# Kernel optimization log

Measured on AMD Instinct MI355X. Metric: run time of the kernel, lower is better.

Reference implementation:

```python
import jax, jax.numpy as jnp
import numpy as np

B, L, V, DIN, H = 256, 256, 2048, 128, 256   # trees, leaves/tree, vocab, in_dim, mem_dim
NODES = 2 * L - 1                            # perfect binary tree, level-by-level layout
LEVELS = int(np.log2(L)) + 1                 # 9 levels: 256,128,...,1 nodes


def setup_inputs() -> dict:
    key = jax.random.key(0)
    ks = jax.random.split(key, 32)
    w = lambda k, shape: jax.random.normal(k, shape, jnp.float32) * 0.05
    inp = {
        "input_ids": jax.random.randint(ks[0], (B, NODES), 0, V),
        "emb": w(ks[1], (V, DIN)),
        # iou projections (i,o,u concatenated -> 3H)
        "Wioux": w(ks[2], (DIN, 3 * H)), "bioux": jnp.zeros((3 * H,), jnp.float32),
        "Wiouh1": w(ks[3], (H, 3 * H)), "biouh1": jnp.zeros((3 * H,), jnp.float32),
        "Wiouh2": w(ks[4], (H, 3 * H)), "biouh2": jnp.zeros((3 * H,), jnp.float32),
        # forget gates
        "Wfx": w(ks[5], (DIN, H)), "bfx": jnp.zeros((H,), jnp.float32),
        "Wfh11": w(ks[6], (H, H)), "bfh11": jnp.zeros((H,), jnp.float32),
        "Wfh12": w(ks[7], (H, H)), "bfh12": jnp.zeros((H,), jnp.float32),
        "Wfh21": w(ks[8], (H, H)), "bfh21": jnp.zeros((H,), jnp.float32),
        "Wfh22": w(ks[9], (H, H)), "bfh22": jnp.zeros((H,), jnp.float32),
        # classifier head
        "Wl1": w(ks[10], (H, 100)), "bl1": jnp.zeros((100,), jnp.float32),
        "Wl2": w(ks[11], (100, 1)), "bl2": jnp.zeros((1,), jnp.float32),
    }
    return inp


def reference(input_ids, emb, Wioux, bioux, Wiouh1, biouh1, Wiouh2, biouh2,
              Wfx, bfx, Wfh11, bfh11, Wfh12, bfh12, Wfh21, bfh21, Wfh22, bfh22,
              Wl1, bl1, Wl2, bl2):
    emb = emb.at[0].set(0.0)                 # padding_idx=0
    xemb = emb[input_ids]                    # [B, NODES, DIN]

    def cell(x, h1, h2, c1, c2):
        iou = (x @ Wioux + bioux) + (h1 @ Wiouh1 + biouh1) + (h2 @ Wiouh2 + biouh2)
        i, o, u = jnp.split(iou, 3, axis=-1)
        i, o, u = jax.nn.sigmoid(i), jax.nn.sigmoid(o), jnp.tanh(u)
        fx = x @ Wfx + bfx
        f0 = jax.nn.sigmoid((h1 @ Wfh11 + bfh11) + (h2 @ Wfh12 + bfh12) + fx)
        f1 = jax.nn.sigmoid((h1 @ Wfh21 + bfh21) + (h2 @ Wfh22 + bfh22) + fx)
        c = i * u + f0 * c1 + f1 * c2
        h = o * jnp.tanh(c)
        return h, c

    # leaves: zero child states
    z = jnp.zeros((B, L, H), jnp.float32)
    h, c = cell(xemb[:, :L], z, z, z, z)     # [B, L, H]

    off, n = 0, L
    for _ in range(LEVELS - 1):              # fixed small structural loop (8 iters)
        off += n
        n //= 2
        x = xemb[:, off:off + n]             # [B, n, DIN]
        h, c = cell(x, h[:, 0::2], h[:, 1::2], c[:, 0::2], c[:, 1::2])

    root_h = h[:, 0]                         # [B, H]
    hid = root_h @ Wl1 + bl1                 # linear1
    pred = (jax.nn.relu(hid) @ Wl2 + bl2)[..., 0]   # [B], arithmetic head (no softmax)
    return pred
```

## Files before the change

### kernel.cpp

```cpp
#include <hip/hip_runtime.h>
#include <math.h>

#define B_ 256
#define L_ 256
#define V_ 2048
#define DIN_ 128
#define H_ 256
#define NODES_ 511

typedef _Float16 half8 __attribute__((ext_vector_type(8)));
typedef float f32x4 __attribute__((ext_vector_type(4)));

__device__ __forceinline__ float sigm(float x) { return 1.f / (1.f + __expf(-x)); }
__device__ __forceinline__ float tanh_f(float x) {
    float xc = fminf(fmaxf(x, -15.f), 15.f);
    float e = __expf(2.f * xc);
    return (e - 1.f) / (e + 1.f);
}
__device__ __forceinline__ void gload16(const void* g, void* l) {
    __builtin_amdgcn_global_load_lds((const __attribute__((address_space(1))) unsigned int*)g,
                                     (__attribute__((address_space(3))) unsigned int*)l, 16, 0, 0);
}
template<int N> __device__ __forceinline__ void vwaitN() {
    asm volatile("s_waitcnt vmcnt(%0)" :: "i"(N) : "memory");
}

__global__ void build_WTh(_Float16* __restrict__ WTh,
    const float* __restrict__ Wiouh1, const float* __restrict__ Wfh11, const float* __restrict__ Wfh21,
    const float* __restrict__ Wiouh2, const float* __restrict__ Wfh12, const float* __restrict__ Wfh22)
{
    int e = blockIdx.x * 256 + threadIdx.x;
    int nn = e >> 9, k = e & 511;
    int g = nn >> 8, t = nn & 255;
    float v;
    if (k < 256) {
        v = (g < 3) ? Wiouh1[k * 768 + nn] : ((g == 3) ? Wfh11[k * 256 + t] : Wfh21[k * 256 + t]);
    } else {
        int kp = k - 256;
        v = (g < 3) ? Wiouh2[kp * 768 + nn] : ((g == 3) ? Wfh12[kp * 256 + t] : Wfh22[kp * 256 + t]);
    }
    WTh[e] = (_Float16)v;
}

__global__ __launch_bounds__(256) void build_table(float* __restrict__ tab, const float* __restrict__ emb,
    const float* __restrict__ Wioux, const float* __restrict__ Wfx,
    const float* __restrict__ bioux, const float* __restrict__ biouh1, const float* __restrict__ biouh2,
    const float* __restrict__ bfx, const float* __restrict__ bfh11, const float* __restrict__ bfh12,
    const float* __restrict__ bfh21, const float* __restrict__ bfh22)
{
    __shared__ float As[64][33];
    __shared__ float Ws[32][65];
    const int tid = threadIdx.x, tx = tid & 15, ty = tid >> 4;
    const int i0 = blockIdx.x * 64, c0 = blockIdx.y * 64;
    const int g = c0 >> 8;
    float acc[4][4];
    #pragma unroll
    for (int i = 0; i < 4; ++i)
        #pragma unroll
        for (int j = 0; j < 4; ++j) acc[i][j] = 0.f;

    for (int k0 = 0; k0 < 128; k0 += 32) {
        #pragma unroll
        for (int it = 0; it < 2; ++it) {
            int f = tid + it * 256;
            int row = f >> 3, kk = (f & 7) * 4;
            int gr = i0 + row;
            float4 av = (gr == 0) ? make_float4(0.f, 0.f, 0.f, 0.f)
                                  : *(const float4*)(emb + (size_t)gr * 128 + k0 + kk);
            As[row][kk] = av.x; As[row][kk + 1] = av.y; As[row][kk + 2] = av.z; As[row][kk + 3] = av.w;
            int k = f >> 4, cc = (f & 15) * 4;
            int col = c0 + cc;
            float4 wv = (g < 3) ? *(const float4*)(Wioux + (size_t)(k0 + k) * 768 + col)
                                : *(const float4*)(Wfx + (size_t)(k0 + k) * 256 + (col & 255));
            Ws[k][cc] = wv.x; Ws[k][cc + 1] = wv.y; Ws[k][cc + 2] = wv.z; Ws[k][cc + 3] = wv.w;
        }
        __syncthreads();
        #pragma unroll 8
        for (int k = 0; k < 32; ++k) {
            float a[4], w[4];
            #pragma unroll
            for (int i = 0; i < 4; ++i) a[i] = As[ty * 4 + i][k];
            #pragma unroll
            for (int j = 0; j < 4; ++j) w[j] = Ws[k][tx * 4 + j];
            #pragma unroll
            for (int i = 0; i < 4; ++i)
                #pragma unroll
                for (int j = 0; j < 4; ++j) acc[i][j] = fmaf(a[i], w[j], acc[i][j]);
        }
        __syncthreads();
    }
    #pragma unroll
    for (int j = 0; j < 4; ++j) {
        int col = c0 + tx * 4 + j; int t = col & 255;
        float bs = (g < 3) ? (bioux[col] + biouh1[col] + biouh2[col])
                 : (g == 3) ? (bfx[t] + bfh11[t] + bfh12[t])
                            : (bfx[t] + bfh21[t] + bfh22[t]);
        #pragma unroll
        for (int i = 0; i < 4; ++i)
            tab[(size_t)(i0 + ty * 4 + i) * 1280 + col] = acc[i][j] + bs;
    }
}

__global__ void build_h0c0(const float* __restrict__ tab, _Float16* __restrict__ H0h, float* __restrict__ H0c) {
    int id = blockIdx.x, t = threadIdx.x;
    const float* tp = tab + (size_t)id * 1280 + t;
    float vi = sigm(tp[0]), vo = sigm(tp[256]), vu = tanh_f(tp[512]);
    float c = vi * vu;
    H0h[id * 256 + t] = (_Float16)(vo * tanh_f(c));
    H0c[id * 256 + t] = c;
}

template<bool LVL1, int RT>
__global__ __launch_bounds__(256, (RT >= 4 ? 2 : 4)) void cellH(
    const _Float16* __restrict__ WTh, const float* __restrict__ tab,
    const int* __restrict__ ids,
    const _Float16* __restrict__ h_prev, const float* __restrict__ c_prev,
    _Float16* __restrict__ h_out, float* __restrict__ c_out,
    int n, int ln, int off, int nx)
{
    constexpr int BM = RT * 64;
    constexpr int AB = BM * 64;
    __shared__ __align__(16) char Asm[3][AB];
    __shared__ __align__(16) char Bsm[3][5120];
    const int tid = threadIdx.x, lane = tid & 63, wid = tid >> 6;
    const int l15 = lane & 15, lg = lane >> 4;

    int bid = blockIdx.x, x, y;
    if ((nx & 7) == 0) { int xcd = bid & 7, rank = bid >> 3; x = xcd * (nx >> 3) + (rank >> 4); y = rank & 15; }
    else { x = bid >> 4; y = bid & 15; }
    const int rowB = x * BM;
    const int t0 = y * 16;

    const unsigned segOff = (unsigned)((((lane & 3) ^ ((lane >> 3) & 3))) * 16);
    unsigned srcA[RT], srcB1_[LVL1 ? RT : 1];
    #pragma unroll
    for (int i = 0; i < RT; ++i) {
        int rl = (wid * RT + i) * 16 + (lane >> 2);
        int r = rowB + rl;
        if constexpr (LVL1) {
            int b = r >> 7, j2 = r & 127;
            srcA[i]   = (unsigned)ids[b * NODES_ + 2 * j2] * 512u + segOff;
            srcB1_[i] = (unsigned)ids[b * NODES_ + 2 * j2 + 1] * 512u + segOff;
        } else {
            srcA[i] = (unsigned)r * 1024u + segOff;
        }
    }
    unsigned bsrc0, bsrc1 = 0;
    {
        int nr = tid >> 2, j = tid & 3;
        int ng = (nr >> 4) * 256 + t0 + (nr & 15);
        bsrc0 = (unsigned)((ng * 512 + ((j ^ ((nr >> 1) & 3)) * 8)) * 2);
        if (wid == 0) {
            int ng2 = 1024 + t0 + (tid >> 2);
            int seg2 = (tid & 3) ^ ((tid >> 3) & 3);
            bsrc1 = (unsigned)((ng2 * 512 + seg2 * 8) * 2);
        }
    }
    const char* hPB = (const char*)h_prev;
    const char* wPB = (const char*)WTh;

    f32x4 acc[RT][5];
    #pragma unroll
    for (int rt = 0; rt < RT; ++rt)
        #pragma unroll
        for (int g = 0; g < 5; ++g) acc[rt][g] = (f32x4)0.f;

    const int xw = (l15 >> 1) & 3;

    auto STAGE = [&](int st, int buf) {
        #pragma unroll
        for (int i = 0; i < RT; ++i) {
            unsigned sa;
            if constexpr (LVL1)
                sa = (st < 8) ? (srcA[i] + (unsigned)st * 64u) : (srcB1_[i] + (unsigned)(st - 8) * 64u);
            else
                sa = srcA[i] + (unsigned)st * 64u;
            gload16(hPB + sa, &Asm[buf][(wid * RT + i) * 1024 + lane * 16]);
        }
        gload16(wPB + bsrc0 + (unsigned)st * 64u, &Bsm[buf][tid * 16]);
        if (wid == 0) gload16(wPB + bsrc1 + (unsigned)st * 64u, &Bsm[buf][4096 + tid * 16]);
    };
    auto COMPUTE = [&](int buf) {
        half8 aF[RT];
        #pragma unroll
        for (int rt = 0; rt < RT; ++rt)
            aF[rt] = *(const half8*)&Asm[buf][(wid * RT * 16 + rt * 16 + l15) * 64 + ((lg ^ xw) * 16)];
        #pragma unroll
        for (int g = 0; g < 5; ++g) {
            half8 bF = *(const half8*)&Bsm[buf][(g * 16 + l15) * 64 + ((lg ^ xw) * 16)];
            #pragma unroll
            for (int rt = 0; rt < RT; ++rt)
                acc[rt][g] = __builtin_amdgcn_mfma_f32_16x16x32_f16(aF[rt], bF, acc[rt][g], 0, 0, 0);
        }
    };
    auto WAITB = [&](bool counted) {
        if (counted) { if (wid == 0) vwaitN<RT + 2>(); else vwaitN<RT + 1>(); }
        else vwaitN<0>();
        __builtin_amdgcn_s_barrier();
        __builtin_amdgcn_sched_barrier(0);
    };

    STAGE(0, 0);
    STAGE(1, 1);
    WAITB(true);

    #pragma unroll
    for (int S = 0; S < 16; ++S) {
        if (S + 2 < 16) STAGE(S + 2, (S + 2) % 3);
        COMPUTE(S % 3);
        if (S < 15) WAITB(S + 2 < 16);
    }

    const int tcol = t0 + l15;
    #pragma unroll
    for (int rt = 0; rt < RT; ++rt) {
        #pragma unroll
        for (int q = 0; q < 4; ++q) {
            int row = rowB + wid * (RT * 16) + rt * 16 + lg * 4 + q;
            int b = row >> ln, j = row & (n - 1);
            int id = ids[b * NODES_ + off + j];
            const float* tp = tab + (size_t)id * 1280 + tcol;
            float c1, c2;
            if constexpr (LVL1) {
                int bb = row >> 7, jj = row & 127;
                c1 = c_prev[(size_t)ids[bb * NODES_ + 2 * jj] * 256 + tcol];
                c2 = c_prev[(size_t)ids[bb * NODES_ + 2 * jj + 1] * 256 + tcol];
            } else {
                const float* cpp = c_prev + (size_t)row * 512 + tcol;
                c1 = cpp[0]; c2 = cpp[256];
            }
            float vi  = sigm(acc[rt][0][q] + tp[0]);
            float vo  = sigm(acc[rt][1][q] + tp[256]);
            float vu  = tanh_f(acc[rt][2][q] + tp[512]);
            float vf0 = sigm(acc[rt][3][q] + tp[768]);
            float vf1 = sigm(acc[rt][4][q] + tp[1024]);
            float c = vi * vu + vf0 * c1 + vf1 * c2;
            size_t ob = (size_t)row * 256 + tcol;
            h_out[ob] = (_Float16)(vo * tanh_f(c));
            c_out[ob] = c;
        }
    }
}

__global__ void head_kernel(const _Float16* __restrict__ hroot,
    const float* __restrict__ Wl1, const float* __restrict__ bl1,
    const float* __restrict__ Wl2, const float* __restrict__ bl2,
    float* __restrict__ out)
{
    __shared__ float hrow[H_];
    __shared__ float red[256];
    int b = blockIdx.x; int tid = threadIdx.x;
    hrow[tid] = (float)hroot[(size_t)b * H_ + tid];
    __syncthreads();
    float v = 0.f;
    if (tid < 100) {
        float s = bl1[tid];
        for (int k = 0; k < H_; ++k) s = fmaf(hrow[k], Wl1[k * 100 + tid], s);
        v = fmaxf(s, 0.f) * Wl2[tid];
    }
    red[tid] = v;
    __syncthreads();
    for (int s = 128; s > 0; s >>= 1) { if (tid < s) red[tid] += red[tid + s]; __syncthreads(); }
    if (tid == 0) out[b] = red[0] + bl2[0];
}

extern "C" void kernel_launch(void* const* d_in, const int* in_sizes, int n_in,
                              void* d_out, int out_size, void* d_ws, size_t ws_size,
                              hipStream_t stream) {
    const int*   ids    = (const int*)d_in[0];
    const float* emb    = (const float*)d_in[1];
    const float* Wioux  = (const float*)d_in[2];
    const float* bioux  = (const float*)d_in[3];
    const float* Wiouh1 = (const float*)d_in[4];
    const float* biouh1 = (const float*)d_in[5];
    const float* Wiouh2 = (const float*)d_in[6];
    const float* biouh2 = (const float*)d_in[7];
    const float* Wfx    = (const float*)d_in[8];
    const float* bfx    = (const float*)d_in[9];
    const float* Wfh11  = (const float*)d_in[10];
    const float* bfh11  = (const float*)d_in[11];
    const float* Wfh12  = (const float*)d_in[12];
    const float* bfh12  = (const float*)d_in[13];
    const float* Wfh21  = (const float*)d_in[14];
    const float* bfh21  = (const float*)d_in[15];
    const float* Wfh22  = (const float*)d_in[16];
    const float* bfh22  = (const float*)d_in[17];
    const float* Wl1    = (const float*)d_in[18];
    const float* bl1    = (const float*)d_in[19];
    const float* Wl2    = (const float*)d_in[20];
    const float* bl2    = (const float*)d_in[21];
    float* out = (float*)d_out;

    char* wsb = (char*)d_ws;
    _Float16* WTh = (_Float16*)(wsb);
    float*    tab = (float*)(wsb + 1310720);
    _Float16* H0h = (_Float16*)(wsb + 11796480);
    float*    H0c = (float*)(wsb + 12845056);
    _Float16* hA  = (_Float16*)(wsb + 14942208);
    _Float16* hB  = (_Float16*)(wsb + 23330816);
    float*    cA  = (float*)(wsb + 40108032);
    float*    cB  = (float*)(wsb + 56885248);

    build_WTh<<<dim3(2560), 256, 0, stream>>>(WTh, Wiouh1, Wfh11, Wfh21, Wiouh2, Wfh12, Wfh22);
    build_table<<<dim3(32, 20), 256, 0, stream>>>(tab, emb, Wioux, Wfx,
        bioux, biouh1, biouh2, bfx, bfh11, bfh12, bfh21, bfh22);
    build_h0c0<<<dim3(2048), 256, 0, stream>>>(tab, H0h, H0c);

    cellH<true, 4><<<dim3(2048), 256, 0, stream>>>(WTh, tab, ids, H0h, H0c, hB, cB, 128, 7, 256, 128);

    _Float16 *hp = hB, *hn = hA;
    float    *cp = cB, *cn = cA;
    int off = 384, n = 64, ln = 6;
    for (int lvl = 2; lvl <= 8; ++lvl) {
        int M = B_ * n;
        if (M >= 2048) {
            int nx = M / 256;
            cellH<false, 4><<<dim3(nx * 16), 256, 0, stream>>>(WTh, tab, ids, hp, cp, hn, cn, n, ln, off, nx);
        } else if (M >= 1024) {
            int nx = M / 128;
            cellH<false, 2><<<dim3(nx * 16), 256, 0, stream>>>(WTh, tab, ids, hp, cp, hn, cn, n, ln, off, nx);
        } else {
            int nx = M / 64;
            cellH<false, 1><<<dim3(nx * 16), 256, 0, stream>>>(WTh, tab, ids, hp, cp, hn, cn, n, ln, off, nx);
        }
        off += n; n >>= 1; --ln;
        _Float16* t1 = hp; hp = hn; hn = t1;
        float*    t2 = cp; cp = cn; cn = t2;
    }

    head_kernel<<<dim3(256), 256, 0, stream>>>(hp, Wl1, bl1, Wl2, bl2, out);
}
```

Before: 278.0 us.

## Fold embedding projection into cell GEMM instead of gathering precomputed table

Internal cell kernels no longer gather per-vocab precomputed x-projections (1280 floats per node) from a table. Instead they stage fp16 embeddings as four extra K-steps of the MFMA GEMM, using a combined 640-wide weight matrix and a summed bias vector. This replaces a scattered fp32 epilogue gather with 25% more GEMM work per cell and new prep kernels. The old table is still built for the leaf level.

```diff
diff --git a/kernel.cpp b/kernel.cpp
--- a/kernel.cpp
+++ b/kernel.cpp
@@ -25,21 +25,45 @@
     asm volatile("s_waitcnt vmcnt(%0)" :: "i"(N) : "memory");
 }
 
-__global__ void build_WTh(_Float16* __restrict__ WTh,
+__global__ void build_WT(_Float16* __restrict__ WT,
+    const float* __restrict__ Wioux, const float* __restrict__ Wfx,
     const float* __restrict__ Wiouh1, const float* __restrict__ Wfh11, const float* __restrict__ Wfh21,
     const float* __restrict__ Wiouh2, const float* __restrict__ Wfh12, const float* __restrict__ Wfh22)
 {
     int e = blockIdx.x * 256 + threadIdx.x;
-    int nn = e >> 9, k = e & 511;
+    int nn = e / 640, k = e - nn * 640;
     int g = nn >> 8, t = nn & 255;
     float v;
-    if (k < 256) {
-        v = (g < 3) ? Wiouh1[k * 768 + nn] : ((g == 3) ? Wfh11[k * 256 + t] : Wfh21[k * 256 + t]);
+    if (k < 128) {
+        v = (g < 3) ? Wioux[k * 768 + nn] : Wfx[k * 256 + t];
+    } else if (k < 384) {
+        int kp = k - 128;
+        v = (g < 3) ? Wiouh1[kp * 768 + nn] : ((g == 3) ? Wfh11[kp * 256 + t] : Wfh21[kp * 256 + t]);
     } else {
-        int kp = k - 256;
+        int kp = k - 384;
         v = (g < 3) ? Wiouh2[kp * 768 + nn] : ((g == 3) ? Wfh12[kp * 256 + t] : Wfh22[kp * 256 + t]);
     }
-    WTh[e] = (_Float16)v;
+    WT[e] = (_Float16)v;
+}
+
+__global__ void build_bias(float* __restrict__ bias,
+    const float* __restrict__ bioux, const float* __restrict__ biouh1, const float* __restrict__ biouh2,
+    const float* __restrict__ bfx, const float* __restrict__ bfh11, const float* __restrict__ bfh12,
+    const float* __restrict__ bfh21, const float* __restrict__ bfh22)
+{
+    int e = blockIdx.x * 256 + threadIdx.x;
+    if (e >= 1280) return;
+    int g = e >> 8, t = e & 255;
+    float v;
+    if (g < 3)       v = bioux[e] + biouh1[e] + biouh2[e];
+    else if (g == 3) v = bfx[t] + bfh11[t] + bfh12[t];
+    else             v = bfx[t] + bfh21[t] + bfh22[t];
+    bias[e] = v;
+}
+
+__global__ void build_embh(_Float16* __restrict__ EH, const float* __restrict__ emb) {
+    int e = blockIdx.x * 256 + threadIdx.x;
+    EH[e] = (e < DIN_) ? (_Float16)0.f : (_Float16)emb[e];
 }
 
 __global__ __launch_bounds__(256) void build_table(float* __restrict__ tab, const float* __restrict__ emb,
@@ -111,16 +135,15 @@
 }
 
 template<bool LVL1, int RT>
-__global__ __launch_bounds__(256, (RT >= 4 ? 2 : 4)) void cellH(
-    const _Float16* __restrict__ WTh, const float* __restrict__ tab,
-    const int* __restrict__ ids,
+__global__ __launch_bounds__(256, (RT >= 4 ? 2 : 4)) void cellJ(
+    const _Float16* __restrict__ WT, const float* __restrict__ bias,
+    const _Float16* __restrict__ embh, const int* __restrict__ ids,
     const _Float16* __restrict__ h_prev, const float* __restrict__ c_prev,
     _Float16* __restrict__ h_out, float* __restrict__ c_out,
     int n, int ln, int off, int nx)
 {
     constexpr int BM = RT * 64;
-    constexpr int AB = BM * 64;
-    __shared__ __align__(16) char Asm[3][AB];
+    __shared__ __align__(16) char Asm[3][BM * 64];
     __shared__ __align__(16) char Bsm[3][5120];
     const int tid = threadIdx.x, lane = tid & 63, wid = tid >> 6;
     const int l15 = lane & 15, lg = lane >> 4;
@@ -132,15 +155,17 @@
     const int t0 = y * 16;
 
     const unsigned segOff = (unsigned)((((lane & 3) ^ ((lane >> 3) & 3))) * 16);
-    unsigned srcA[RT], srcB1_[LVL1 ? RT : 1];
+    unsigned srcX[RT], srcA[RT], srcB1_[LVL1 ? RT : 1];
     #pragma unroll
     for (int i = 0; i < RT; ++i) {
         int rl = (wid * RT + i) * 16 + (lane >> 2);
         int r = rowB + rl;
+        int b = r >> ln, j = r & (n - 1);
+        srcX[i] = (unsigned)ids[b * NODES_ + off + j] * 256u + segOff;
         if constexpr (LVL1) {
-            int b = r >> 7, j2 = r & 127;
-            srcA[i]   = (unsigned)ids[b * NODES_ + 2 * j2] * 512u + segOff;
-            srcB1_[i] = (unsigned)ids[b * NODES_ + 2 * j2 + 1] * 512u + segOff;
+            int bb = r >> 7, jj = r & 127;
+            srcA[i]   = (unsigned)ids[bb * NODES_ + 2 * jj] * 512u + segOff;
+            srcB1_[i] = (unsigned)ids[bb * NODES_ + 2 * jj + 1] * 512u + segOff;
         } else {
             srcA[i] = (unsigned)r * 1024u + segOff;
         }
@@ -149,15 +174,16 @@
     {
         int nr = tid >> 2, j = tid & 3;
         int ng = (nr >> 4) * 256 + t0 + (nr & 15);
-        bsrc0 = (unsigned)((ng * 512 + ((j ^ ((nr >> 1) & 3)) * 8)) * 2);
+        bsrc0 = (unsigned)((ng * 640 + ((j ^ ((nr >> 1) & 3)) * 8)) * 2);
         if (wid == 0) {
             int ng2 = 1024 + t0 + (tid >> 2);
             int seg2 = (tid & 3) ^ ((tid >> 3) & 3);
-            bsrc1 = (unsigned)((ng2 * 512 + seg2 * 8) * 2);
+            bsrc1 = (unsigned)((ng2 * 640 + seg2 * 8) * 2);
         }
     }
     const char* hPB = (const char*)h_prev;
-    const char* wPB = (const char*)WTh;
+    const char* xPB = (const char*)embh;
+    const char* wPB = (const char*)WT;
 
     f32x4 acc[RT][5];
     #pragma unroll
@@ -170,12 +196,14 @@
     auto STAGE = [&](int st, int buf) {
         #pragma unroll
         for (int i = 0; i < RT; ++i) {
-            unsigned sa;
-            if constexpr (LVL1)
-                sa = (st < 8) ? (srcA[i] + (unsigned)st * 64u) : (srcB1_[i] + (unsigned)(st - 8) * 64u);
-            else
-                sa = srcA[i] + (unsigned)st * 64u;
-            gload16(hPB + sa, &Asm[buf][(wid * RT + i) * 1024 + lane * 16]);
+            const char* bp; unsigned sa;
+            if (st < 4) { bp = xPB; sa = srcX[i] + (unsigned)st * 64u; }
+            else if constexpr (LVL1) {
+                bp = hPB;
+                sa = (st < 12) ? (srcA[i] + (unsigned)(st - 4) * 64u)
+                               : (srcB1_[i] + (unsigned)(st - 12) * 64u);
+            } else { bp = hPB; sa = srcA[i] + (unsigned)(st - 4) * 64u; }
+            gload16(bp + sa, &Asm[buf][(wid * RT + i) * 1024 + lane * 16]);
         }
         gload16(wPB + bsrc0 + (unsigned)st * 64u, &Bsm[buf][tid * 16]);
         if (wid == 0) gload16(wPB + bsrc1 + (unsigned)st * 64u, &Bsm[buf][4096 + tid * 16]);
@@ -205,21 +233,20 @@
     WAITB(true);
 
     #pragma unroll
-    for (int S = 0; S < 16; ++S) {
-        if (S + 2 < 16) STAGE(S + 2, (S + 2) % 3);
+    for (int S = 0; S < 20; ++S) {
+        if (S + 2 < 20) STAGE(S + 2, (S + 2) % 3);
         COMPUTE(S % 3);
-        if (S < 15) WAITB(S + 2 < 16);
+        if (S < 19) WAITB(S + 2 < 20);
     }
 
     const int tcol = t0 + l15;
+    const float b0 = bias[tcol], b1 = bias[256 + tcol], b2 = bias[512 + tcol];
+    const float b3 = bias[768 + tcol], b4 = bias[1024 + tcol];
     #pragma unroll
     for (int rt = 0; rt < RT; ++rt) {
         #pragma unroll
         for (int q = 0; q < 4; ++q) {
             int row = rowB + wid * (RT * 16) + rt * 16 + lg * 4 + q;
-            int b = row >> ln, j = row & (n - 1);
-            int id = ids[b * NODES_ + off + j];
-            const float* tp = tab + (size_t)id * 1280 + tcol;
             float c1, c2;
             if constexpr (LVL1) {
                 int bb = row >> 7, jj = row & 127;
@@ -229,11 +256,11 @@
                 const float* cpp = c_prev + (size_t)row * 512 + tcol;
                 c1 = cpp[0]; c2 = cpp[256];
             }
-            float vi  = sigm(acc[rt][0][q] + tp[0]);
-            float vo  = sigm(acc[rt][1][q] + tp[256]);
-            float vu  = tanh_f(acc[rt][2][q] + tp[512]);
-            float vf0 = sigm(acc[rt][3][q] + tp[768]);
-            float vf1 = sigm(acc[rt][4][q] + tp[1024]);
+            float vi  = sigm(acc[rt][0][q] + b0);
+            float vo  = sigm(acc[rt][1][q] + b1);
+            float vu  = tanh_f(acc[rt][2][q] + b2);
+            float vf0 = sigm(acc[rt][3][q] + b3);
+            float vf1 = sigm(acc[rt][4][q] + b4);
             float c = vi * vu + vf0 * c1 + vf1 * c2;
             size_t ob = (size_t)row * 256 + tcol;
             h_out[ob] = (_Float16)(vo * tanh_f(c));
@@ -292,21 +319,25 @@
     float* out = (float*)d_out;
 
     char* wsb = (char*)d_ws;
-    _Float16* WTh = (_Float16*)(wsb);
-    float*    tab = (float*)(wsb + 1310720);
-    _Float16* H0h = (_Float16*)(wsb + 11796480);
-    float*    H0c = (float*)(wsb + 12845056);
-    _Float16* hA  = (_Float16*)(wsb + 14942208);
-    _Float16* hB  = (_Float16*)(wsb + 23330816);
-    float*    cA  = (float*)(wsb + 40108032);
-    float*    cB  = (float*)(wsb + 56885248);
-
-    build_WTh<<<dim3(2560), 256, 0, stream>>>(WTh, Wiouh1, Wfh11, Wfh21, Wiouh2, Wfh12, Wfh22);
+    _Float16* WT   = (_Float16*)(wsb);
+    _Float16* embh = (_Float16*)(wsb + 1638400);
+    float*    bias = (float*)(wsb + 2162688);
+    float*    tab  = (float*)(wsb + 2167808);
+    _Float16* H0h  = (_Float16*)(wsb + 12653568);
+    float*    H0c  = (float*)(wsb + 13702144);
+    _Float16* hA   = (_Float16*)(wsb + 15799296);
+    _Float16* hB   = (_Float16*)(wsb + 24187904);
+    float*    cA   = (float*)(wsb + 40965120);
+    float*    cB   = (float*)(wsb + 57742336);
+
+    build_WT<<<dim3(3200), 256, 0, stream>>>(WT, Wioux, Wfx, Wiouh1, Wfh11, Wfh21, Wiouh2, Wfh12, Wfh22);
+    build_bias<<<dim3(5), 256, 0, stream>>>(bias, bioux, biouh1, biouh2, bfx, bfh11, bfh12, bfh21, bfh22);
+    build_embh<<<dim3(1024), 256, 0, stream>>>(embh, emb);
     build_table<<<dim3(32, 20), 256, 0, stream>>>(tab, emb, Wioux, Wfx,
         bioux, biouh1, biouh2, bfx, bfh11, bfh12, bfh21, bfh22);
     build_h0c0<<<dim3(2048), 256, 0, stream>>>(tab, H0h, H0c);
 
-    cellH<true, 4><<<dim3(2048), 256, 0, stream>>>(WTh, tab, ids, H0h, H0c, hB, cB, 128, 7, 256, 128);
+    cellJ<true, 4><<<dim3(2048), 256, 0, stream>>>(WT, bias, embh, ids, H0h, H0c, hB, cB, 128, 7, 256, 128);
 
     _Float16 *hp = hB, *hn = hA;
     float    *cp = cB, *cn = cA;
@@ -315,13 +346,13 @@
         int M = B_ * n;
         if (M >= 2048) {
             int nx = M / 256;
-            cellH<false, 4><<<dim3(nx * 16), 256, 0, stream>>>(WTh, tab, ids, hp, cp, hn, cn, n, ln, off, nx);
+            cellJ<false, 4><<<dim3(nx * 16), 256, 0, stream>>>(WT, bias, embh, ids, hp, cp, hn, cn, n, ln, off, nx);
         } else if (M >= 1024) {
             int nx = M / 128;
-            cellH<false, 2><<<dim3(nx * 16), 256, 0, stream>>>(WTh, tab, ids, hp, cp, hn, cn, n, ln, off, nx);
+            cellJ<false, 2><<<dim3(nx * 16), 256, 0, stream>>>(WT, bias, embh, ids, hp, cp, hn, cn, n, ln, off, nx);
         } else {
             int nx = M / 64;
-            cellH<false, 1><<<dim3(nx * 16), 256, 0, stream>>>(WTh, tab, ids, hp, cp, hn, cn, n, ln, off, nx);
+            cellJ<false, 1><<<dim3(nx * 16), 256, 0, stream>>>(WT, bias, embh, ids, hp, cp, hn, cn, n, ln, off, nx);
         }
         off += n; n >>= 1; --ln;
         _Float16* t1 = hp; hp = hn; hn = t1;
```

Result: no change. 278.2 us (+0.1%).
